# Kernel optimization log

Hardware: AMD Instinct MI355X
Metric: run time of the kernel (lower is better)

The kernel has to match this reference:

```python
import jax, jax.numpy as jnp
import numpy as np


def setup_inputs() -> dict:
    key = jax.random.key(0)
    ks = jax.random.split(key, 11)
    B, N, C, E, O = 16, 2048, 64, 16, 64
    H, M, K = 16, 2, 2  # hyperGNN_dim, middle_dim, cheb_k
    s = 0.1
    return {
        "x": jax.random.normal(ks[0], (B, N, C), dtype=jnp.float32),
        "emb0": jax.random.normal(ks[1], (B, N, E), dtype=jnp.float32),
        "emb1": jax.random.normal(ks[2], (N, E), dtype=jnp.float32),
        "w1": jax.random.normal(ks[3], (C, H), dtype=jnp.float32) * s,
        "b1": jnp.zeros((H,), dtype=jnp.float32),
        "w2": jax.random.normal(ks[4], (H, M), dtype=jnp.float32) * s,
        "b2": jnp.zeros((M,), dtype=jnp.float32),
        "w3": jax.random.normal(ks[5], (M, E), dtype=jnp.float32) * s,
        "b3": jnp.zeros((E,), dtype=jnp.float32),
        "weights_pool": jax.random.normal(ks[6], (E, K, C, O), dtype=jnp.float32) * s,
        "bias_pool": jax.random.normal(ks[7], (E, O), dtype=jnp.float32) * s,
    }


def reference(x, emb0, emb1, w1, b1, w2, b2, w3, b3, weights_pool, bias_pool):
    # hypernetwork MLP: Linear -> sigmoid -> Linear -> sigmoid -> Linear
    h = jax.nn.sigmoid(x @ w1 + b1)
    h = jax.nn.sigmoid(h @ w2 + b2)
    filt = h @ w3 + b3                                   # (B,N,E)
    nodevec = jnp.tanh(emb0 * filt)                      # (B,N,E)
    # dynamic adjacency: relu(nodevec @ nodevec^T)
    adj = jax.nn.relu(jnp.einsum('bnd,bmd->bnm', nodevec, nodevec))  # (B,N,N)
    # normalized Laplacian: D^{-1/2} A D^{-1/2} (diag_embed expressed via broadcast)
    d = jnp.sum(adj, axis=-1) ** (-0.5)                  # (B,N)
    L = d[:, :, None] * adj * d[:, None, :]              # (B,N,N)
    # supports1 is identity -> x_g1 == x
    x_g1 = x
    x_g2 = jnp.einsum('bnm,bmc->bnc', L, x)
    x_g = jnp.stack([x_g1, x_g2], axis=2)                # (B,N,K=2,C)
    # per-node hypernetwork weights and bias
    weights = jnp.einsum('nd,dkio->nkio', emb1, weights_pool)  # (N,K,C,O)
    bias = emb1 @ bias_pool                               # (N,O)
    out = jnp.einsum('bnki,nkio->bno', x_g, weights) + bias
    return out
```

## Files before the change

### kernel.cpp

```cpp
#include <hip/hip_runtime.h>
#include <hip/hip_bf16.h>

#define B_ 16
#define N_ 2048
#define C_ 64
#define E_ 16
#define O_ 64
#define H_ 16

typedef __attribute__((ext_vector_type(8)))  short short8;
typedef __attribute__((ext_vector_type(16))) float f32x16;

#define NVB_OFF   0u
#define RSP_OFF   262144u
#define XST_OFF   327680u
#define YT_OFF    1376256u
#define XGALL_OFF 5570560u
#define WPB_OFF   7667712u
#define E1B_OFF   7733760u

__device__ __forceinline__ unsigned short f2bf(float f) {
  union { float f; unsigned int u; } v; v.f = f;
  unsigned int r = v.u + 0x7FFFu + ((v.u >> 16) & 1u);
  return (unsigned short)(r >> 16);
}

#define CVT_PK(dst, lo_, hi_) \
  asm("v_cvt_pk_bf16_f32 %0, %1, %2" : "=v"(dst) : "v"(lo_), "v"(hi_))
#define PL_SWAP(x_, y_) \
  asm("v_permlane32_swap_b32 %0, %1" : "+v"(x_), "+v"(y_))

__global__ __launch_bounds__(256) void k0_prep(
    const float* __restrict__ wp, const float* __restrict__ bp,
    const float* __restrict__ emb1,
    unsigned short* __restrict__ wpB, unsigned short* __restrict__ emb1b)
{
  int id = blockIdx.x * 256 + threadIdx.x;
  if (id < 132096) {
    int t = id & 7, o = (id >> 3) & 63, rest = id >> 9;
    int sub = rest & 1, kc = rest >> 1;
    int q2 = sub * 8 + t;
    float v = (kc < 128) ? wp[(size_t)(kc * 16 + q2) * 64 + o]
                         : bp[(size_t)q2 * 64 + o];
    wpB[id] = f2bf(v);
  } else {
    int id2 = id - 132096;
    emb1b[id2] = f2bf(emb1[id2]);
  }
}

__global__ __launch_bounds__(256) void k1_hyper(
    const float* __restrict__ x, const float* __restrict__ emb0,
    const float* __restrict__ w1, const float* __restrict__ b1,
    const float* __restrict__ w2, const float* __restrict__ b2,
    const float* __restrict__ w3, const float* __restrict__ b3,
    unsigned short* __restrict__ nvb, unsigned short* __restrict__ xgall)
{
  __shared__ float w1s[C_*H_];
  __shared__ float b1s[H_], w2s[H_*2], b2s[2], w3s[2*E_], b3s[E_];
  int tid = threadIdx.x;
  for (int i = tid; i < C_*H_; i += 256) w1s[i] = w1[i];
  if (tid < H_)   b1s[tid] = b1[tid];
  if (tid < H_*2) w2s[tid] = w2[tid];
  if (tid < 2)    b2s[tid] = b2[tid];
  if (tid < 2*E_) w3s[tid] = w3[tid];
  if (tid < E_)   b3s[tid] = b3[tid];
  __syncthreads();

  int idx = blockIdx.x * 256 + tid;
  float xr[C_];
  const float4* xp = reinterpret_cast<const float4*>(x + (size_t)idx * C_);
  #pragma unroll
  for (int j = 0; j < 16; ++j) {
    float4 v = xp[j];
    xr[4*j] = v.x; xr[4*j+1] = v.y; xr[4*j+2] = v.z; xr[4*j+3] = v.w;
  }
  unsigned short xus[C_];
  #pragma unroll
  for (int c = 0; c < C_; ++c) xus[c] = f2bf(xr[c]);
  unsigned short* xo = xgall + (size_t)idx * 128;
  #pragma unroll
  for (int j = 0; j < 8; ++j)
    reinterpret_cast<uint4*>(xo)[j] = reinterpret_cast<uint4*>(xus)[j];

  float h1[H_];
  #pragma unroll
  for (int h = 0; h < H_; ++h) h1[h] = b1s[h];
  #pragma unroll 8
  for (int c = 0; c < C_; ++c) {
    float xv = xr[c];
    #pragma unroll
    for (int j = 0; j < 4; ++j) {
      float4 w = reinterpret_cast<const float4*>(&w1s[c*H_])[j];
      h1[4*j]   = fmaf(xv, w.x, h1[4*j]);
      h1[4*j+1] = fmaf(xv, w.y, h1[4*j+1]);
      h1[4*j+2] = fmaf(xv, w.z, h1[4*j+2]);
      h1[4*j+3] = fmaf(xv, w.w, h1[4*j+3]);
    }
  }
  #pragma unroll
  for (int h = 0; h < H_; ++h) h1[h] = 1.f / (1.f + __expf(-h1[h]));
  float a0 = b2s[0], a1 = b2s[1];
  #pragma unroll
  for (int h = 0; h < H_; ++h) {
    a0 = fmaf(h1[h], w2s[h*2],   a0);
    a1 = fmaf(h1[h], w2s[h*2+1], a1);
  }
  a0 = 1.f / (1.f + __expf(-a0));
  a1 = 1.f / (1.f + __expf(-a1));

  const float4* ep = reinterpret_cast<const float4*>(emb0 + (size_t)idx * E_);
  unsigned short us[E_];
  #pragma unroll
  for (int j = 0; j < 4; ++j) {
    float4 e = ep[j];
    int c = 4*j;
    us[c]   = f2bf(tanhf(e.x * (b3s[c]   + a0*w3s[c]   + a1*w3s[E_+c])));
    us[c+1] = f2bf(tanhf(e.y * (b3s[c+1] + a0*w3s[c+1] + a1*w3s[E_+c+1])));
    us[c+2] = f2bf(tanhf(e.z * (b3s[c+2] + a0*w3s[c+2] + a1*w3s[E_+c+2])));
    us[c+3] = f2bf(tanhf(e.w * (b3s[c+3] + a0*w3s[c+3] + a1*w3s[E_+c+3])));
  }
  *reinterpret_cast<short8*>(nvb + (size_t)idx * E_)     = *reinterpret_cast<short8*>(&us[0]);
  *reinterpret_cast<short8*>(nvb + (size_t)idx * E_ + 8) = *reinterpret_cast<short8*>(&us[8]);
}

__global__ __launch_bounds__(256) void p1_rowsum(
    const unsigned short* __restrict__ nvb, float* __restrict__ rsp)
{
  int tid = threadIdx.x, lane = tid & 63, wid = tid >> 6;
  int lo = lane & 31, hi = lane >> 5;
  int orig = blockIdx.x;
  int eff = (orig & 7) * 64 + (orig >> 3);
  int rb = eff & 15, b = (eff >> 4) & 15, part = eff >> 8;
  int N0 = rb * 128 + wid * 32;

  short8 bfrag = *reinterpret_cast<const short8*>(
      nvb + ((size_t)b * N_ + N0 + lo) * E_ + 8 * hi);
  f32x16 zero = {};
  float rs = 0.f;
  const unsigned short* abase =
      nvb + ((size_t)b * N_ + part * 1024 + lo) * E_ + 8 * hi;
  #pragma unroll 2
  for (int mc = 0; mc < 32; ++mc) {
    short8 afrag = *reinterpret_cast<const short8*>(abase + (size_t)mc * 32 * E_);
    f32x16 p = __builtin_amdgcn_mfma_f32_32x32x16_bf16(afrag, bfrag, zero, 0, 0, 0);
    #pragma unroll
    for (int r = 0; r < 16; ++r) rs += fmaxf(p[r], 0.f);
  }
  rs += __shfl_xor(rs, 32, 64);
  if (lane < 32) rsp[((size_t)part * B_ + b) * N_ + N0 + lo] = rs;
}

__global__ __launch_bounds__(256) void p2_scaleT(
    const float* __restrict__ x, const float* __restrict__ rsp,
    unsigned short* __restrict__ xsT)
{
  int tid = threadIdx.x;
  int c = tid & 63, g = tid >> 6;
  int m0 = blockIdx.x * 128 + g * 32;
  int b  = blockIdx.y;
  const float* rp = rsp + (size_t)b * N_;
  unsigned int pk[16];
  #pragma unroll
  for (int k = 0; k < 32; ++k) {
    int m = m0 + k;
    float d = rsqrtf(rp[m] + rp[(size_t)B_ * N_ + m]);
    float v = d * x[((size_t)b * N_ + m) * C_ + c];
    unsigned short us = f2bf(v);
    if (k & 1) pk[k >> 1] |= ((unsigned int)us) << 16;
    else       pk[k >> 1]  = us;
  }
  unsigned short* o = xsT + ((size_t)b * C_ + c) * N_ + m0;
  #pragma unroll
  for (int j = 0; j < 4; ++j)
    reinterpret_cast<uint4*>(o)[j] = *reinterpret_cast<uint4*>(&pk[4*j]);
}

__global__ __launch_bounds__(256) void p3_spmm(
    const unsigned short* __restrict__ nvb, const unsigned short* __restrict__ xsT,
    float* __restrict__ yT)
{
  int tid = threadIdx.x, lane = tid & 63, wid = tid >> 6;
  int lo = lane & 31, hi = lane >> 5;
  int orig = blockIdx.x;
  int eff = (orig & 7) * 64 + (orig >> 3);
  int rb = eff & 15, b = (eff >> 4) & 15, part = eff >> 8;
  int N0 = rb * 128 + wid * 32;

  short8 bfrag = *reinterpret_cast<const short8*>(
      nvb + ((size_t)b * N_ + N0 + lo) * E_ + 8 * hi);
  f32x16 acc0 = {}, acc1 = {};
  f32x16 zero = {};
  const unsigned short* abase =
      nvb + ((size_t)b * N_ + part * 1024 + lo) * E_ + 8 * hi;
  const unsigned short* xb0 = xsT + ((size_t)b * C_ + lo) * N_ + part * 1024 + 8 * hi;
  const unsigned short* xb1 = xb0 + (size_t)32 * N_;

  #pragma unroll 2
  for (int mc = 0; mc < 32; ++mc) {
    int mo = mc * 32;
    short8 afrag = *reinterpret_cast<const short8*>(abase + (size_t)mo * E_);
    short8 x00 = *reinterpret_cast<const short8*>(xb0 + mo);
    short8 x01 = *reinterpret_cast<const short8*>(xb0 + mo + 16);
    short8 x10 = *reinterpret_cast<const short8*>(xb1 + mo);
    short8 x11 = *reinterpret_cast<const short8*>(xb1 + mo + 16);

    f32x16 p = __builtin_amdgcn_mfma_f32_32x32x16_bf16(afrag, bfrag, zero, 0, 0, 0);
    float q[16];
    #pragma unroll
    for (int r = 0; r < 16; ++r) q[r] = fmaxf(p[r], 0.f);

    unsigned int A0, Bb0, C0, D0, A1, Bb1, C1, D1;
    CVT_PK(A0,  q[0],  q[1]);  CVT_PK(Bb0, q[2],  q[3]);
    CVT_PK(C0,  q[4],  q[5]);  CVT_PK(D0,  q[6],  q[7]);
    CVT_PK(A1,  q[8],  q[9]);  CVT_PK(Bb1, q[10], q[11]);
    CVT_PK(C1,  q[12], q[13]); CVT_PK(D1,  q[14], q[15]);
    PL_SWAP(A0, C0);  PL_SWAP(Bb0, D0);
    PL_SWAP(A1, C1);  PL_SWAP(Bb1, D1);

    union { unsigned int u[4]; short8 s; } f0, f1;
    f0.u[0] = A0; f0.u[1] = Bb0; f0.u[2] = C0; f0.u[3] = D0;
    f1.u[0] = A1; f1.u[1] = Bb1; f1.u[2] = C1; f1.u[3] = D1;

    acc0 = __builtin_amdgcn_mfma_f32_32x32x16_bf16(x00, f0.s, acc0, 0, 0, 0);
    acc0 = __builtin_amdgcn_mfma_f32_32x32x16_bf16(x01, f1.s, acc0, 0, 0, 0);
    acc1 = __builtin_amdgcn_mfma_f32_32x32x16_bf16(x10, f0.s, acc1, 0, 0, 0);
    acc1 = __builtin_amdgcn_mfma_f32_32x32x16_bf16(x11, f1.s, acc1, 0, 0, 0);
  }

  float* yb = yT + ((size_t)part * B_ + b) * C_ * N_;
  #pragma unroll
  for (int r = 0; r < 16; ++r) {
    int cl = (r & 3) + 8 * (r >> 2) + 4 * hi;
    yb[(size_t)cl * N_ + N0 + lo]        = acc0[r];
    yb[(size_t)(cl + 32) * N_ + N0 + lo] = acc1[r];
  }
}

__global__ __launch_bounds__(256) void p4_xg2(
    const float* __restrict__ yT, const float* __restrict__ rsp,
    unsigned short* __restrict__ xgall)
{
  __shared__ unsigned short tile[64][72];
  int tid = threadIdx.x;
  int nl = tid & 63, cg = tid >> 6;
  int n0 = blockIdx.x * 64, b = blockIdx.y;
  int n = n0 + nl;
  float rs = rsp[(size_t)b * N_ + n] + rsp[(size_t)(B_*N_) + (size_t)b * N_ + n];
  float dn = rsqrtf(rs);
  const float* y0 = yT + (size_t)b * C_ * N_;
  const size_t PST = (size_t)B_ * C_ * N_;
  #pragma unroll
  for (int cc = 0; cc < 16; cc += 2) {
    int c = cg * 16 + cc;
    float v0 = y0[(size_t)c * N_ + n]     + y0[PST + (size_t)c * N_ + n];
    float v1 = y0[(size_t)(c+1) * N_ + n] + y0[PST + (size_t)(c+1) * N_ + n];
    unsigned int pk = (unsigned int)f2bf(dn * v0) | ((unsigned int)f2bf(dn * v1) << 16);
    *reinterpret_cast<unsigned int*>(&tile[nl][c]) = pk;
  }
  __syncthreads();
  int q = tid & 3, j = tid >> 2;
  uint4 va = *reinterpret_cast<const uint4*>(&tile[j][q*16]);
  uint4 vb = *reinterpret_cast<const uint4*>(&tile[j][q*16 + 8]);
  unsigned short* o = xgall + ((size_t)b * N_ + n0 + j) * 128 + 64 + q * 16;
  *reinterpret_cast<uint4*>(o)     = va;
  *reinterpret_cast<uint4*>(o + 8) = vb;
}

__global__ __launch_bounds__(256) void k5_out(
    const unsigned short* __restrict__ xgall, const unsigned short* __restrict__ emb1b,
    const float* __restrict__ emb1, const unsigned short* __restrict__ wpB,
    float* __restrict__ out)
{
  int tid = threadIdx.x, lane = tid & 63, wid = tid >> 6;
  int lo = lane & 31, hi = lane >> 5;
  int gw = blockIdx.x * 4 + wid;
  int mt = gw >> 1;
  int o0 = (gw & 1) * 32;
  int M0 = mt * 32;
  int n0 = M0 & (N_ - 1);

  const unsigned short* arow = xgall + (size_t)(M0 + lo) * 128 + 8 * hi;
  short8 a[8];
  #pragma unroll
  for (int c8 = 0; c8 < 8; ++c8)
    a[c8] = *reinterpret_cast<const short8*>(arow + c8 * 16);
  short8 abias = *reinterpret_cast<const short8*>(
      emb1b + (size_t)(n0 + lo) * E_ + 8 * hi);

  f32x16 acc = {};
  f32x16 kzero = {};

  int nr[16];
  #pragma unroll
  for (int r = 0; r < 16; ++r) nr[r] = n0 + (r & 3) + 8 * (r >> 2) + 4 * hi;

  #pragma unroll 2
  for (int dg = 0; dg < 8; ++dg) {
    float2 e2[16];
    #pragma unroll
    for (int r = 0; r < 16; ++r)
      e2[r] = *reinterpret_cast<const float2*>(emb1 + (size_t)nr[r] * E_ + dg * 2);
    #pragma unroll
    for (int dd = 0; dd < 2; ++dd) {
      int d = dg * 2 + dd;
      const unsigned short* bbase = wpB + ((size_t)((d * 8) * 2 + hi) * 64 + o0 + lo) * 8;
      f32x16 t0 = kzero, t1 = kzero;
      #pragma unroll
      for (int c8 = 0; c8 < 8; c8 += 2) {
        short8 B0 = *reinterpret_cast<const short8*>(bbase + (size_t)(c8    ) * 1024);
        short8 B1 = *reinterpret_cast<const short8*>(bbase + (size_t)(c8 + 1) * 1024);
        t0 = __builtin_amdgcn_mfma_f32_32x32x16_bf16(a[c8],     B0, t0, 0, 0, 0);
        t1 = __builtin_amdgcn_mfma_f32_32x32x16_bf16(a[c8 + 1], B1, t1, 0, 0, 0);
      }
      #pragma unroll
      for (int r = 0; r < 16; ++r) {
        float e = dd ? e2[r].y : e2[r].x;
        acc[r] = fmaf(e, t0[r] + t1[r], acc[r]);
      }
    }
  }
  {
    const unsigned short* bbase = wpB + ((size_t)(256 + hi) * 64 + o0 + lo) * 8;
    short8 Bb = *reinterpret_cast<const short8*>(bbase);
    acc = __builtin_amdgcn_mfma_f32_32x32x16_bf16(abias, Bb, acc, 0, 0, 0);
  }
  #pragma unroll
  for (int r = 0; r < 16; ++r) {
    int cl = (r & 3) + 8 * (r >> 2) + 4 * hi;
    out[(size_t)(M0 + cl) * O_ + o0 + lo] = acc[r];
  }
}

extern "C" void kernel_launch(void* const* d_in, const int* in_sizes, int n_in,
                              void* d_out, int out_size, void* d_ws, size_t ws_size,
                              hipStream_t stream)
{
  const float* x    = (const float*)d_in[0];
  const float* emb0 = (const float*)d_in[1];
  const float* emb1 = (const float*)d_in[2];
  const float* w1   = (const float*)d_in[3];
  const float* b1   = (const float*)d_in[4];
  const float* w2   = (const float*)d_in[5];
  const float* b2   = (const float*)d_in[6];
  const float* w3   = (const float*)d_in[7];
  const float* b3   = (const float*)d_in[8];
  const float* wp   = (const float*)d_in[9];
  const float* bp   = (const float*)d_in[10];
  float* out = (float*)d_out;
  float* ws  = (float*)d_ws;

  unsigned short* nvb   = (unsigned short*)(ws + NVB_OFF);
  float*          rsp   = ws + RSP_OFF;
  unsigned short* xsT   = (unsigned short*)(ws + XST_OFF);
  float*          yT    = ws + YT_OFF;
  unsigned short* xgall = (unsigned short*)(ws + XGALL_OFF);
  unsigned short* wpB   = (unsigned short*)(ws + WPB_OFF);
  unsigned short* emb1b = (unsigned short*)(ws + E1B_OFF);

  k0_prep  <<<644, 256, 0, stream>>>(wp, bp, emb1, wpB, emb1b);
  k1_hyper <<<128, 256, 0, stream>>>(x, emb0, w1, b1, w2, b2, w3, b3, nvb, xgall);
  p1_rowsum<<<512, 256, 0, stream>>>(nvb, rsp);
  p2_scaleT<<<dim3(16,16), 256, 0, stream>>>(x, rsp, xsT);
  p3_spmm  <<<512, 256, 0, stream>>>(nvb, xsT, yT);
  p4_xg2   <<<dim3(32,16), 256, 0, stream>>>(yT, rsp, xgall);
  k5_out   <<<512, 256, 0, stream>>>(xgall, emb1b, emb1, wpB, out);
}
```

Baseline: 185.8 us.

## Split rowsum and spmm reductions into four parts and tile xsT layout

The column dimension of the rowsum and spmm kernels is now split into four partial parts instead of two, doubling the grid to 1024 blocks with occupancy hints. The scaled-x buffer is re-laid out into 32-column tiles so each spmm iteration reads a contiguous chunk. Consumers now sum four partial row sums and four partial yT buffers, which doubles the yT workspace and the reduction traffic in p4 in exchange for more parallelism.

```diff
diff --git a/kernel.cpp b/kernel.cpp
--- a/kernel.cpp
+++ b/kernel.cpp
@@ -13,11 +13,11 @@
 
 #define NVB_OFF   0u
 #define RSP_OFF   262144u
-#define XST_OFF   327680u
-#define YT_OFF    1376256u
-#define XGALL_OFF 5570560u
-#define WPB_OFF   7667712u
-#define E1B_OFF   7733760u
+#define XST_OFF   393216u
+#define YT_OFF    1441792u
+#define XGALL_OFF 9830400u
+#define WPB_OFF   11927552u
+#define E1B_OFF   11993600u
 
 __device__ __forceinline__ unsigned short f2bf(float f) {
   union { float f; unsigned int u; } v; v.f = f;
@@ -124,13 +124,13 @@
   *reinterpret_cast<short8*>(nvb + (size_t)idx * E_ + 8) = *reinterpret_cast<short8*>(&us[8]);
 }
 
-__global__ __launch_bounds__(256) void p1_rowsum(
+__global__ __launch_bounds__(256, 4) void p1_rowsum(
     const unsigned short* __restrict__ nvb, float* __restrict__ rsp)
 {
   int tid = threadIdx.x, lane = tid & 63, wid = tid >> 6;
   int lo = lane & 31, hi = lane >> 5;
   int orig = blockIdx.x;
-  int eff = (orig & 7) * 64 + (orig >> 3);
+  int eff = (orig & 7) * 128 + (orig >> 3);
   int rb = eff & 15, b = (eff >> 4) & 15, part = eff >> 8;
   int N0 = rb * 128 + wid * 32;
 
@@ -139,9 +139,9 @@
   f32x16 zero = {};
   float rs = 0.f;
   const unsigned short* abase =
-      nvb + ((size_t)b * N_ + part * 1024 + lo) * E_ + 8 * hi;
+      nvb + ((size_t)b * N_ + part * 512 + lo) * E_ + 8 * hi;
   #pragma unroll 2
-  for (int mc = 0; mc < 32; ++mc) {
+  for (int mc = 0; mc < 16; ++mc) {
     short8 afrag = *reinterpret_cast<const short8*>(abase + (size_t)mc * 32 * E_);
     f32x16 p = __builtin_amdgcn_mfma_f32_32x32x16_bf16(afrag, bfrag, zero, 0, 0, 0);
     #pragma unroll
@@ -160,30 +160,32 @@
   int m0 = blockIdx.x * 128 + g * 32;
   int b  = blockIdx.y;
   const float* rp = rsp + (size_t)b * N_;
+  const size_t RST = (size_t)B_ * N_;
   unsigned int pk[16];
   #pragma unroll
   for (int k = 0; k < 32; ++k) {
     int m = m0 + k;
-    float d = rsqrtf(rp[m] + rp[(size_t)B_ * N_ + m]);
+    float s = rp[m] + rp[RST + m] + rp[2*RST + m] + rp[3*RST + m];
+    float d = rsqrtf(s);
     float v = d * x[((size_t)b * N_ + m) * C_ + c];
     unsigned short us = f2bf(v);
     if (k & 1) pk[k >> 1] |= ((unsigned int)us) << 16;
     else       pk[k >> 1]  = us;
   }
-  unsigned short* o = xsT + ((size_t)b * C_ + c) * N_ + m0;
+  unsigned short* o = xsT + (((size_t)b * 64 + (m0 >> 5)) * 64 + c) * 32;
   #pragma unroll
   for (int j = 0; j < 4; ++j)
     reinterpret_cast<uint4*>(o)[j] = *reinterpret_cast<uint4*>(&pk[4*j]);
 }
 
-__global__ __launch_bounds__(256) void p3_spmm(
+__global__ __launch_bounds__(256, 4) void p3_spmm(
     const unsigned short* __restrict__ nvb, const unsigned short* __restrict__ xsT,
     float* __restrict__ yT)
 {
   int tid = threadIdx.x, lane = tid & 63, wid = tid >> 6;
   int lo = lane & 31, hi = lane >> 5;
   int orig = blockIdx.x;
-  int eff = (orig & 7) * 64 + (orig >> 3);
+  int eff = (orig & 7) * 128 + (orig >> 3);
   int rb = eff & 15, b = (eff >> 4) & 15, part = eff >> 8;
   int N0 = rb * 128 + wid * 32;
 
@@ -192,18 +194,18 @@
   f32x16 acc0 = {}, acc1 = {};
   f32x16 zero = {};
   const unsigned short* abase =
-      nvb + ((size_t)b * N_ + part * 1024 + lo) * E_ + 8 * hi;
-  const unsigned short* xb0 = xsT + ((size_t)b * C_ + lo) * N_ + part * 1024 + 8 * hi;
-  const unsigned short* xb1 = xb0 + (size_t)32 * N_;
+      nvb + ((size_t)b * N_ + part * 512 + lo) * E_ + 8 * hi;
+  const unsigned short* xtile =
+      xsT + (((size_t)b * 64 + part * 16) * 64) * 32 + lo * 32 + 8 * hi;
 
   #pragma unroll 2
-  for (int mc = 0; mc < 32; ++mc) {
-    int mo = mc * 32;
-    short8 afrag = *reinterpret_cast<const short8*>(abase + (size_t)mo * E_);
-    short8 x00 = *reinterpret_cast<const short8*>(xb0 + mo);
-    short8 x01 = *reinterpret_cast<const short8*>(xb0 + mo + 16);
-    short8 x10 = *reinterpret_cast<const short8*>(xb1 + mo);
-    short8 x11 = *reinterpret_cast<const short8*>(xb1 + mo + 16);
+  for (int mc = 0; mc < 16; ++mc) {
+    short8 afrag = *reinterpret_cast<const short8*>(abase + (size_t)mc * 32 * E_);
+    const unsigned short* xt = xtile + (size_t)mc * 2048;
+    short8 x00 = *reinterpret_cast<const short8*>(xt);
+    short8 x01 = *reinterpret_cast<const short8*>(xt + 16);
+    short8 x10 = *reinterpret_cast<const short8*>(xt + 1024);
+    short8 x11 = *reinterpret_cast<const short8*>(xt + 1024 + 16);
 
     f32x16 p = __builtin_amdgcn_mfma_f32_32x32x16_bf16(afrag, bfrag, zero, 0, 0, 0);
     float q[16];
@@ -246,15 +248,18 @@
   int nl = tid & 63, cg = tid >> 6;
   int n0 = blockIdx.x * 64, b = blockIdx.y;
   int n = n0 + nl;
-  float rs = rsp[(size_t)b * N_ + n] + rsp[(size_t)(B_*N_) + (size_t)b * N_ + n];
+  const size_t RST = (size_t)B_ * N_;
+  float rs = rsp[(size_t)b * N_ + n]       + rsp[RST + (size_t)b * N_ + n]
+           + rsp[2*RST + (size_t)b * N_ + n] + rsp[3*RST + (size_t)b * N_ + n];
   float dn = rsqrtf(rs);
   const float* y0 = yT + (size_t)b * C_ * N_;
   const size_t PST = (size_t)B_ * C_ * N_;
   #pragma unroll
   for (int cc = 0; cc < 16; cc += 2) {
     int c = cg * 16 + cc;
-    float v0 = y0[(size_t)c * N_ + n]     + y0[PST + (size_t)c * N_ + n];
-    float v1 = y0[(size_t)(c+1) * N_ + n] + y0[PST + (size_t)(c+1) * N_ + n];
+    size_t o0 = (size_t)c * N_ + n, o1 = (size_t)(c+1) * N_ + n;
+    float v0 = y0[o0] + y0[PST + o0] + y0[2*PST + o0] + y0[3*PST + o0];
+    float v1 = y0[o1] + y0[PST + o1] + y0[2*PST + o1] + y0[3*PST + o1];
     unsigned int pk = (unsigned int)f2bf(dn * v0) | ((unsigned int)f2bf(dn * v1) << 16);
     *reinterpret_cast<unsigned int*>(&tile[nl][c]) = pk;
   }
@@ -360,9 +365,9 @@
 
   k0_prep  <<<644, 256, 0, stream>>>(wp, bp, emb1, wpB, emb1b);
   k1_hyper <<<128, 256, 0, stream>>>(x, emb0, w1, b1, w2, b2, w3, b3, nvb, xgall);
-  p1_rowsum<<<512, 256, 0, stream>>>(nvb, rsp);
+  p1_rowsum<<<1024, 256, 0, stream>>>(nvb, rsp);
   p2_scaleT<<<dim3(16,16), 256, 0, stream>>>(x, rsp, xsT);
-  p3_spmm  <<<512, 256, 0, stream>>>(nvb, xsT, yT);
+  p3_spmm  <<<1024, 256, 0, stream>>>(nvb, xsT, yT);
   p4_xg2   <<<dim3(32,16), 256, 0, stream>>>(yT, rsp, xgall);
   k5_out   <<<512, 256, 0, stream>>>(xgall, emb1b, emb1, wpB, out);
 }
```

Result: faster. 178.5 us (-4.0%).
